# Kernel optimization log

Measured on AMD Instinct MI355X. Metric: run time of the kernel, lower is better.

The kernel has to match this reference:

```python
import jax, jax.numpy as jnp
import numpy as np

EMB_DIM = 1024
NUM_HEADS = 16
HEAD_DIM = EMB_DIM // NUM_HEADS


def _theta_vector(head_dim):
    # theta_i = 10000^(-2i/head_dim), i = 0..head_dim/2-1 (standard RoPE)
    i = jnp.arange(head_dim // 2, dtype=jnp.float32)
    return jnp.power(10000.0, -2.0 * i / head_dim)


def _apply_rope(x, cos, sin):
    # x: [B,S,H,D]; cos,sin: [B,S,1,D/2]. Pairwise 2x2 rotation per dim-pair.
    B, S, H, D = x.shape
    xp = x.reshape(B, S, H, D // 2, 2)
    x0, x1 = xp[..., 0], xp[..., 1]
    r0 = x0 * cos - x1 * sin
    r1 = x0 * sin + x1 * cos
    return jnp.stack([r0, r1], axis=-1).reshape(B, S, H, D)


def setup_inputs() -> dict:
    key = jax.random.key(0)
    ks = jax.random.split(key, 11)
    B, S = 2, 2048
    sc = 1.0 / np.sqrt(EMB_DIM)
    x = jax.random.normal(ks[0], (B, S, EMB_DIM), dtype=jnp.float32)
    positions = jnp.sort(jax.random.randint(ks[1], (B, S), 0, 8192), axis=-1)
    Wq = jax.random.normal(ks[2], (EMB_DIM, EMB_DIM), dtype=jnp.float32) * sc
    bq = jax.random.normal(ks[3], (EMB_DIM,), dtype=jnp.float32) * 0.01
    Wk = jax.random.normal(ks[4], (EMB_DIM, EMB_DIM), dtype=jnp.float32) * sc
    bk = jax.random.normal(ks[5], (EMB_DIM,), dtype=jnp.float32) * 0.01
    Wv = jax.random.normal(ks[6], (EMB_DIM, EMB_DIM), dtype=jnp.float32) * sc
    bv = jax.random.normal(ks[7], (EMB_DIM,), dtype=jnp.float32) * 0.01
    Wo = jax.random.normal(ks[8], (EMB_DIM, EMB_DIM), dtype=jnp.float32) * sc
    bo = jax.random.normal(ks[9], (EMB_DIM,), dtype=jnp.float32) * 0.01
    return {"x": x, "positions": positions, "Wq": Wq, "bq": bq, "Wk": Wk,
            "bk": bk, "Wv": Wv, "bv": bv, "Wo": Wo, "bo": bo}


def reference(x, positions, Wq, bq, Wk, bk, Wv, bv, Wo, bo):
    B, S, E = x.shape
    H, D = NUM_HEADS, HEAD_DIM
    Q = (x @ Wq + bq).reshape(B, S, H, D)
    K = (x @ Wk + bk).reshape(B, S, H, D)
    V = (x @ Wv + bv).reshape(B, S, H, D)
    theta = _theta_vector(D)                       # [D/2]
    ang = positions.astype(jnp.float32)[..., None] * theta  # [B,S,D/2]
    cos = jnp.cos(ang)[:, :, None, :]              # [B,S,1,D/2]
    sin = jnp.sin(ang)[:, :, None, :]
    Qr = _apply_rope(Q, cos, sin).transpose(0, 2, 1, 3)   # [B,H,S,D]
    Kr = _apply_rope(K, cos, sin).transpose(0, 2, 1, 3)
    Vh = V.transpose(0, 2, 1, 3)
    scores = jnp.einsum('bhqd,bhkd->bhqk', Qr, Kr) / jnp.sqrt(jnp.float32(D))
    probs = jax.nn.softmax(scores, axis=-1)
    ctx = jnp.einsum('bhqk,bhkd->bhqd', probs, Vh)
    ctx = ctx.transpose(0, 2, 1, 3).reshape(B, S, E)
    return ctx @ Wo + bo
```

## Files before the change

kernel.cpp:

```cpp
#include <hip/hip_runtime.h>
#include <hip/hip_bf16.h>
#include <math.h>

#define B_ 2
#define S_ 2048
#define E_ 1024
#define H_ 16
#define D_ 64
#define M_ 4096
#define NT2 32
#define KVB 64

typedef __bf16 bf16;
typedef __bf16 bf16x4 __attribute__((ext_vector_type(4)));
typedef __bf16 bf16x8 __attribute__((ext_vector_type(8)));
typedef float f32x4 __attribute__((ext_vector_type(4)));
typedef float f32x16 __attribute__((ext_vector_type(16)));

__device__ __forceinline__ void gload_lds16(const void* g, void* lds) {
  __builtin_amdgcn_global_load_lds(
      (const __attribute__((address_space(1))) unsigned int*)g,
      (__attribute__((address_space(3))) unsigned int*)lds, 16, 0, 0);
}

#define MFMA16(a, b, c) __builtin_amdgcn_mfma_f32_16x16x32_bf16(a, b, c, 0, 0, 0)
#define MFMA32(a, b, c) __builtin_amdgcn_mfma_f32_32x32x16_bf16(a, b, c, 0, 0, 0)

__global__ __launch_bounds__(256)
void split_f32_kernel(const float* __restrict__ in, bf16* __restrict__ hi,
                      bf16* __restrict__ lo, int n4) {
  int i = blockIdx.x * 256 + threadIdx.x;
  if (i >= n4) return;
  float4 v = ((const float4*)in)[i];
  bf16 h0 = (bf16)v.x, h1 = (bf16)v.y, h2 = (bf16)v.z, h3 = (bf16)v.w;
  bf16x4 hv = {h0, h1, h2, h3};
  bf16x4 lv = {(bf16)(v.x - (float)h0), (bf16)(v.y - (float)h1),
               (bf16)(v.z - (float)h2), (bf16)(v.w - (float)h3)};
  *(bf16x4*)(hi + 4 * (size_t)i) = hv;
  *(bf16x4*)(lo + 4 * (size_t)i) = lv;
}

__global__ __launch_bounds__(256)
void transpose_split_kernel(const float* __restrict__ W, bf16* __restrict__ Th,
                            bf16* __restrict__ Tl) {
  __shared__ float tile[32][33];
  const int tx = threadIdx.x & 31, ty = threadIdx.x >> 5;
  const int c0 = blockIdx.x * 32, r0 = blockIdx.y * 32;
#pragma unroll
  for (int i = 0; i < 4; ++i)
    tile[ty + 8 * i][tx] = W[(size_t)(r0 + ty + 8 * i) * E_ + c0 + tx];
  __syncthreads();
#pragma unroll
  for (int i = 0; i < 4; ++i) {
    int rr = ty + 8 * i;
    float v = tile[tx][rr];
    bf16 hv = (bf16)v;
    size_t oidx = (size_t)(c0 + rr) * E_ + r0 + tx;
    Th[oidx] = hv;
    Tl[oidx] = (bf16)(v - (float)hv);
  }
}

__global__ __launch_bounds__(256)
void rope_tab_kernel(const int* __restrict__ pos, float* __restrict__ cosT,
                     float* __restrict__ sinT) {
  int idx = blockIdx.x * 256 + threadIdx.x;
  int t = idx & 31, bs = idx >> 5;
  double th = pow(10000.0, -(double)(2 * t) / 64.0);
  float ang = (float)pos[bs] * (float)th;
  double a = (double)ang;
  cosT[idx] = (float)cos(a);
  sinT[idx] = (float)sin(a);
}

#define BMg 128
#define BNg 128
#define BKg 32

__global__ __launch_bounds__(256)
void gemm_qkv_kernel(const bf16* __restrict__ Ah_g, const bf16* __restrict__ Al_g,
                     const bf16* __restrict__ BhQ, const bf16* __restrict__ BlQ,
                     const bf16* __restrict__ BhK, const bf16* __restrict__ BlK,
                     const bf16* __restrict__ BhV, const bf16* __restrict__ BlV,
                     const float* __restrict__ bqp, const float* __restrict__ bkp,
                     const float* __restrict__ bvp,
                     const float* __restrict__ cosT, const float* __restrict__ sinT,
                     bf16* __restrict__ Qh, bf16* __restrict__ Qlo,
                     bf16* __restrict__ Kh, bf16* __restrict__ Klo,
                     bf16* __restrict__ VTb) {
  __shared__ bf16 lA_h[BMg * BKg], lA_l[BMg * BKg];
  __shared__ bf16 lB_h[BNg * BKg], lB_l[BNg * BKg];
  const int tid = threadIdx.x;
  const int nb = blockIdx.x;
  const int third = nb >> 3;
  const int n0 = (nb & 7) * BNg;
  const int m0 = blockIdx.y * BMg;
  const bf16* Bh_g = third == 0 ? BhQ : third == 1 ? BhK : BhV;
  const bf16* Bl_g = third == 0 ? BlQ : third == 1 ? BlK : BlV;
  const float* bias = third == 0 ? bqp : third == 1 ? bkp : bvp;
  const int wave = tid >> 6, lane = tid & 63;
  const int wr = wave >> 1, wc = wave & 1;
  const int r = lane & 31, half = lane >> 5;
  const int KD = 1024;

  f32x16 acc[2][2] = {};

  for (int kt = 0; kt < KD / BKg; ++kt) {
    const int k0 = kt * BKg;
    {
      const bf16* gsrc[4] = {Ah_g, Al_g, Bh_g, Bl_g};
      bf16* ldst[4] = {lA_h, lA_l, lB_h, lB_l};
      const int rs[4] = {m0, m0, n0, n0};
#pragma unroll
      for (int mm = 0; mm < 4; ++mm) {
#pragma unroll
        for (int i = 0; i < 2; ++i) {
          int c = i * 256 + tid;
          int row = c >> 2, u = c & 3;
          int us = u ^ ((row >> 1) & 3);
          const char* gp =
              (const char*)(gsrc[mm] + (size_t)(rs[mm] + row) * KD + k0) + us * 16;
          char* lp = (char*)ldst[mm] + (size_t)(i * 256 + wave * 64) * 16;
          gload_lds16(gp, lp);
        }
      }
    }
    __syncthreads();
#pragma unroll
    for (int ks = 0; ks < 2; ++ks) {
      bf16x8 a_h[2], a_l[2], b_h[2], b_l[2];
#pragma unroll
      for (int mi = 0; mi < 2; ++mi) {
        int row = wr * 64 + mi * 32 + r;
        int boff = row * 64 + ((ks * 32 + half * 16) ^ (((row >> 1) & 3) << 4));
        a_h[mi] = *(const bf16x8*)((const char*)lA_h + boff);
        a_l[mi] = *(const bf16x8*)((const char*)lA_l + boff);
      }
#pragma unroll
      for (int ni = 0; ni < 2; ++ni) {
        int row = wc * 64 + ni * 32 + r;
        int boff = row * 64 + ((ks * 32 + half * 16) ^ (((row >> 1) & 3) << 4));
        b_h[ni] = *(const bf16x8*)((const char*)lB_h + boff);
        b_l[ni] = *(const bf16x8*)((const char*)lB_l + boff);
      }
#pragma unroll
      for (int mi = 0; mi < 2; ++mi)
#pragma unroll
        for (int ni = 0; ni < 2; ++ni) {
          acc[mi][ni] = MFMA32(a_h[mi], b_h[ni], acc[mi][ni]);
          acc[mi][ni] = MFMA32(a_h[mi], b_l[ni], acc[mi][ni]);
          acc[mi][ni] = MFMA32(a_l[mi], b_h[ni], acc[mi][ni]);
        }
    }
    __syncthreads();
  }

#pragma unroll
  for (int mi = 0; mi < 2; ++mi)
#pragma unroll
    for (int ni = 0; ni < 2; ++ni) {
      const int gcol = n0 + wc * 64 + ni * 32 + r;
      const float bv = bias[gcol];
      if (third < 2) {
        bf16* outH = third == 0 ? Qh : Kh;
        bf16* outL = third == 0 ? Qlo : Klo;
        const int h = gcol >> 6, d = gcol & 63, tt = d >> 1;
#pragma unroll
        for (int tq = 0; tq < 4; ++tq) {
#pragma unroll
          for (int u = 0; u < 4; ++u) {
            int reg = tq * 4 + u;
            int grow = m0 + wr * 64 + mi * 32 + (u + 8 * tq + 4 * half);
            int s = grow & (S_ - 1), b = grow >> 11;
            float v = acc[mi][ni][reg] + bv;
            float other = __shfl_xor(v, 1);
            float cs = cosT[(size_t)(b * S_ + s) * NT2 + tt];
            float sn = sinT[(size_t)(b * S_ + s) * NT2 + tt];
            float vr = (d & 1) ? (other * sn + v * cs) : (v * cs - other * sn);
            if (third == 0) vr *= 0.125f;
            bf16 hv = (bf16)vr;
            bf16 lv = (bf16)(vr - (float)hv);
            size_t idx = (((size_t)(b * H_ + h)) * S_ + s) * D_ + d;
            outH[idx] = hv;
            outL[idx] = lv;
          }
        }
      } else {
        const int h = gcol >> 6, d = gcol & 63;
#pragma unroll
        for (int tq = 0; tq < 4; ++tq) {
          int grow = m0 + wr * 64 + mi * 32 + (8 * tq + 4 * half);
          int s = grow & (S_ - 1), b = grow >> 11;
          ushort4 pk;
          unsigned short* pp = (unsigned short*)&pk;
#pragma unroll
          for (int u = 0; u < 4; ++u) {
            float v = acc[mi][ni][tq * 4 + u] + bv;
            bf16 hv = (bf16)v;
            pp[u] = __builtin_bit_cast(unsigned short, hv);
          }
          *(ushort4*)((unsigned short*)VTb +
                      (((size_t)(b * H_ + h)) * D_ + d) * S_ + s) = pk;
        }
      }
    }
}

__global__ __launch_bounds__(256)
void gemm_o_kernel(const bf16* __restrict__ Ah_g, const bf16* __restrict__ Al_g,
                   const bf16* __restrict__ Bh_g, const bf16* __restrict__ Bl_g,
                   const float* __restrict__ bias, float* __restrict__ outF) {
  __shared__ bf16 lA_h[BMg * BKg], lA_l[BMg * BKg];
  __shared__ bf16 lB_h[BNg * BKg], lB_l[BNg * BKg];
  const int tid = threadIdx.x;
  const int m0 = blockIdx.y * BMg, n0 = blockIdx.x * BNg;
  const int wave = tid >> 6, lane = tid & 63;
  const int wr = wave >> 1, wc = wave & 1;
  const int r = lane & 31, half = lane >> 5;
  const int KD = 1024;

  f32x16 acc[2][2] = {};

  for (int kt = 0; kt < KD / BKg; ++kt) {
    const int k0 = kt * BKg;
    {
      const bf16* gsrc[4] = {Ah_g, Al_g, Bh_g, Bl_g};
      bf16* ldst[4] = {lA_h, lA_l, lB_h, lB_l};
      const int rs[4] = {m0, m0, n0, n0};
#pragma unroll
      for (int mm = 0; mm < 4; ++mm) {
#pragma unroll
        for (int i = 0; i < 2; ++i) {
          int c = i * 256 + tid;
          int row = c >> 2, u = c & 3;
          int us = u ^ ((row >> 1) & 3);
          const char* gp =
              (const char*)(gsrc[mm] + (size_t)(rs[mm] + row) * KD + k0) + us * 16;
          char* lp = (char*)ldst[mm] + (size_t)(i * 256 + wave * 64) * 16;
          gload_lds16(gp, lp);
        }
      }
    }
    __syncthreads();
#pragma unroll
    for (int ks = 0; ks < 2; ++ks) {
      bf16x8 a_h[2], a_l[2], b_h[2], b_l[2];
#pragma unroll
      for (int mi = 0; mi < 2; ++mi) {
        int row = wr * 64 + mi * 32 + r;
        int boff = row * 64 + ((ks * 32 + half * 16) ^ (((row >> 1) & 3) << 4));
        a_h[mi] = *(const bf16x8*)((const char*)lA_h + boff);
        a_l[mi] = *(const bf16x8*)((const char*)lA_l + boff);
      }
#pragma unroll
      for (int ni = 0; ni < 2; ++ni) {
        int row = wc * 64 + ni * 32 + r;
        int boff = row * 64 + ((ks * 32 + half * 16) ^ (((row >> 1) & 3) << 4));
        b_h[ni] = *(const bf16x8*)((const char*)lB_h + boff);
        b_l[ni] = *(const bf16x8*)((const char*)lB_l + boff);
      }
#pragma unroll
      for (int mi = 0; mi < 2; ++mi)
#pragma unroll
        for (int ni = 0; ni < 2; ++ni) {
          acc[mi][ni] = MFMA32(a_h[mi], b_h[ni], acc[mi][ni]);
          acc[mi][ni] = MFMA32(a_h[mi], b_l[ni], acc[mi][ni]);
          acc[mi][ni] = MFMA32(a_l[mi], b_h[ni], acc[mi][ni]);
        }
    }
    __syncthreads();
  }

#pragma unroll
  for (int mi = 0; mi < 2; ++mi)
#pragma unroll
    for (int ni = 0; ni < 2; ++ni) {
      const int gcol = n0 + wc * 64 + ni * 32 + r;
      const float bv = bias[gcol];
#pragma unroll
      for (int tq = 0; tq < 4; ++tq)
#pragma unroll
        for (int u = 0; u < 4; ++u) {
          int grow = m0 + wr * 64 + mi * 32 + (u + 8 * tq + 4 * half);
          outF[(size_t)grow * E_ + gcol] = acc[mi][ni][tq * 4 + u] + bv;
        }
    }
}

__global__ __launch_bounds__(256)
void attn_kernel(const bf16* __restrict__ Qh, const bf16* __restrict__ Ql,
                 const bf16* __restrict__ Kh, const bf16* __restrict__ Kl,
                 const bf16* __restrict__ VT, bf16* __restrict__ Ch,
                 bf16* __restrict__ Cl) {
  __shared__ bf16 sKh[2][KVB * 64];
  __shared__ bf16 sKl[2][KVB * 64];
  __shared__ bf16 sV[2][KVB * 64];

  const int tid = threadIdx.x;
  const int wave = tid >> 6, lane = tid & 63;
  const int r = lane & 15, hq = lane >> 4;
  const int bid = blockIdx.x;
  const int swz = (bid & 7) * 64 + (bid >> 3);
  const int bh = swz >> 4, qblk = swz & 15;
  const int q0 = qblk * 128 + wave * 32;
  const size_t hb = (size_t)bh * (S_ * D_);
  const size_t vb = (size_t)bh * (D_ * S_);

  bf16x8 qh[2][2], ql[2][2];
#pragma unroll
  for (int mi = 0; mi < 2; ++mi)
#pragma unroll
    for (int ks = 0; ks < 2; ++ks) {
      size_t off = hb + (size_t)(q0 + mi * 16 + r) * D_ + ks * 32 + hq * 8;
      qh[mi][ks] = *(const bf16x8*)&Qh[off];
      ql[mi][ks] = *(const bf16x8*)&Ql[off];
    }

  float m_lane[2] = {-1e30f, -1e30f};
  float l_lane[2] = {0.f, 0.f};
  f32x4 o[2][4] = {};

  auto stageK = [&](int kt, int buf) {
    const bf16* kbh = Kh + hb + (size_t)kt * (KVB * D_);
    const bf16* kbl = Kl + hb + (size_t)kt * (KVB * D_);
#pragma unroll
    for (int i = 0; i < 2; ++i) {
      int c = i * 256 + tid;
      int ldo = (i * 256 + wave * 64) * 16;
      int cs = c ^ ((c >> 3) & 7);
      gload_lds16(kbh + cs * 8, (char*)&sKh[buf][0] + ldo);
      gload_lds16(kbl + cs * 8, (char*)&sKl[buf][0] + ldo);
    }
  };
  uint4 vld[2];
  auto loadV = [&](int kt) {
    const bf16* vbp = VT + vb + kt * KVB;
#pragma unroll
    for (int i = 0; i < 2; ++i) {
      int c = i * 256 + tid;
      int row = c >> 3, w = c & 7;
      vld[i] = *(const uint4*)(vbp + (size_t)row * S_ + w * 8);
    }
  };
  auto writeV = [&](int buf) {
#pragma unroll
    for (int i = 0; i < 2; ++i) {
      int c = i * 256 + tid;
      int row = c >> 3, w = c & 7;
      int pb0 = (w >> 2) * 32 + (w & 1) * 16 + ((w >> 1) & 1) * 4;
      char* base = (char*)&sV[buf][0] + row * 128;
      uint2 lo = {vld[i].x, vld[i].y};
      uint2 hi = {vld[i].z, vld[i].w};
      *(uint2*)(base + ((pb0 * 2) ^ ((row & 7) << 4))) = lo;
      *(uint2*)(base + (((pb0 + 8) * 2) ^ ((row & 7) << 4))) = hi;
    }
  };

  stageK(0, 0);
  loadV(0);
  writeV(0);
  __syncthreads();
  int cur = 0;

  for (int kt = 0; kt < S_ / KVB; ++kt) {
    if (kt + 1 < S_ / KVB) {
      stageK(kt + 1, cur ^ 1);
      loadV(kt + 1);
    }

    f32x4 sf[2][4] = {};
#pragma unroll
    for (int nf = 0; nf < 4; ++nf)
#pragma unroll
      for (int ks = 0; ks < 2; ++ks) {
        int kk = nf * 16 + r;
        int boff = (kk * 128 + ks * 64 + hq * 16) ^ ((kk & 7) << 4);
        bf16x8 kkh = *(const bf16x8*)((const char*)&sKh[cur][0] + boff);
        bf16x8 kkl = *(const bf16x8*)((const char*)&sKl[cur][0] + boff);
#pragma unroll
        for (int mi = 0; mi < 2; ++mi) {
          sf[mi][nf] = MFMA16(kkh, qh[mi][ks], sf[mi][nf]);
          sf[mi][nf] = MFMA16(kkh, ql[mi][ks], sf[mi][nf]);
          sf[mi][nf] = MFMA16(kkl, qh[mi][ks], sf[mi][nf]);
        }
      }

    float lmax[2];
#pragma unroll
    for (int mi = 0; mi < 2; ++mi) {
      f32x4 m4;
#pragma unroll
      for (int e = 0; e < 4; ++e)
        m4[e] = fmaxf(fmaxf(sf[mi][0][e], sf[mi][1][e]),
                      fmaxf(sf[mi][2][e], sf[mi][3][e]));
      lmax[mi] = fmaxf(fmaxf(m4[0], m4[1]), fmaxf(m4[2], m4[3]));
    }
    int need = (lmax[0] > m_lane[0] + 8.f) || (lmax[1] > m_lane[1] + 8.f);
    if (__any(need)) {
#pragma unroll
      for (int mi = 0; mi < 2; ++mi) {
        float mx = lmax[mi];
        mx = fmaxf(mx, __shfl_xor(mx, 16));
        mx = fmaxf(mx, __shfl_xor(mx, 32));
        float mn = fmaxf(m_lane[mi], mx);
        float al = __expf(m_lane[mi] - mn);
        l_lane[mi] *= al;
        m_lane[mi] = mn;
        int alb = __builtin_bit_cast(int, al);
#pragma unroll
        for (int j = 0; j < 4; ++j) {
          int g = __builtin_amdgcn_ds_bpermute((hq * 4 + j) * 4, alb);
          float a = __builtin_bit_cast(float, g);
#pragma unroll
          for (int nd = 0; nd < 4; ++nd) o[mi][nd][j] *= a;
        }
      }
    }
    bf16x8 pa[2][2];
#pragma unroll
    for (int mi = 0; mi < 2; ++mi) {
      f32x4 s4 = {};
#pragma unroll
      for (int nf = 0; nf < 4; ++nf)
#pragma unroll
        for (int e = 0; e < 4; ++e) {
          float pv = __expf(sf[mi][nf][e] - m_lane[mi]);
          sf[mi][nf][e] = pv;
          s4[e] += pv;
        }
      l_lane[mi] += s4[0] + s4[1] + s4[2] + s4[3];
#pragma unroll
      for (int ks = 0; ks < 2; ++ks) {
        bf16x8 t;
#pragma unroll
        for (int e = 0; e < 4; ++e) {
          t[e] = (bf16)sf[mi][2 * ks][e];
          t[4 + e] = (bf16)sf[mi][2 * ks + 1][e];
        }
        pa[mi][ks] = t;
      }
    }

#pragma unroll
    for (int nd = 0; nd < 4; ++nd)
#pragma unroll
      for (int ks = 0; ks < 2; ++ks) {
        int dd = nd * 16 + r;
        int boff = (dd * 128 + ks * 64 + hq * 16) ^ ((dd & 7) << 4);
        bf16x8 vv = *(const bf16x8*)((const char*)&sV[cur][0] + boff);
#pragma unroll
        for (int mi = 0; mi < 2; ++mi)
          o[mi][nd] = MFMA16(pa[mi][ks], vv, o[mi][nd]);
      }

    if (kt + 1 < S_ / KVB) writeV(cur ^ 1);
    __syncthreads();
    cur ^= 1;
  }

  const int b = bh >> 4, h = bh & 15;
  float lq[2][4];
#pragma unroll
  for (int mi = 0; mi < 2; ++mi) {
    float lr = l_lane[mi];
    lr += __shfl_xor(lr, 16);
    lr += __shfl_xor(lr, 32);
    int lb = __builtin_bit_cast(int, lr);
#pragma unroll
    for (int j = 0; j < 4; ++j) {
      int g = __builtin_amdgcn_ds_bpermute((hq * 4 + j) * 4, lb);
      lq[mi][j] = __builtin_bit_cast(float, g);
    }
  }
#pragma unroll
  for (int mi = 0; mi < 2; ++mi)
#pragma unroll
    for (int nd = 0; nd < 4; ++nd)
#pragma unroll
      for (int j = 0; j < 4; ++j) {
        int s = q0 + mi * 16 + hq * 4 + j;
        int d = nd * 16 + r;
        float ov = o[mi][nd][j] / lq[mi][j];
        bf16 hv = (bf16)ov;
        bf16 lv = (bf16)(ov - (float)hv);
        size_t idx = (((size_t)(b * S_ + s)) * H_ + h) * D_ + d;
        Ch[idx] = hv;
        Cl[idx] = lv;
      }
}

extern "C" void kernel_launch(void* const* d_in, const int* in_sizes, int n_in,
                              void* d_out, int out_size, void* d_ws, size_t ws_size,
                              hipStream_t stream) {
  const float* x = (const float*)d_in[0];
  const int* pos = (const int*)d_in[1];
  const float* Wq = (const float*)d_in[2];
  const float* bq = (const float*)d_in[3];
  const float* Wk = (const float*)d_in[4];
  const float* bk = (const float*)d_in[5];
  const float* Wv = (const float*)d_in[6];
  const float* bv = (const float*)d_in[7];
  const float* Wo = (const float*)d_in[8];
  const float* bo = (const float*)d_in[9];
  float* out = (float*)d_out;

  char* p = (char*)d_ws;
  auto alloc = [&](size_t bytes) {
    char* rp = p;
    p += (bytes + 255) & ~(size_t)255;
    return rp;
  };
  const size_t XB = (size_t)M_ * E_ * sizeof(bf16);
  const size_t WB = (size_t)E_ * E_ * sizeof(bf16);
  const size_t TB = (size_t)B_ * S_ * NT2 * sizeof(float);
  bf16* Xh = (bf16*)alloc(XB);
  bf16* Xl = (bf16*)alloc(XB);
  bf16* WqTh = (bf16*)alloc(WB); bf16* WqTl = (bf16*)alloc(WB);
  bf16* WkTh = (bf16*)alloc(WB); bf16* WkTl = (bf16*)alloc(WB);
  bf16* WvTh = (bf16*)alloc(WB); bf16* WvTl = (bf16*)alloc(WB);
  bf16* WoTh = (bf16*)alloc(WB); bf16* WoTl = (bf16*)alloc(WB);
  float* cosT = (float*)alloc(TB);
  float* sinT = (float*)alloc(TB);
  bf16* Qh = (bf16*)alloc(XB); bf16* Qlo = (bf16*)alloc(XB);
  bf16* Kh = (bf16*)alloc(XB); bf16* Klo = (bf16*)alloc(XB);
  bf16* VTb = (bf16*)alloc(XB);
  bf16* Ch = Xh;
  bf16* Cl = Xl;

  split_f32_kernel<<<M_ * E_ / 4 / 256, 256, 0, stream>>>(x, Xh, Xl, M_ * E_ / 4);
  dim3 tg(32, 32);
  transpose_split_kernel<<<tg, 256, 0, stream>>>(Wq, WqTh, WqTl);
  transpose_split_kernel<<<tg, 256, 0, stream>>>(Wk, WkTh, WkTl);
  transpose_split_kernel<<<tg, 256, 0, stream>>>(Wv, WvTh, WvTl);
  transpose_split_kernel<<<tg, 256, 0, stream>>>(Wo, WoTh, WoTl);
  rope_tab_kernel<<<B_ * S_ * NT2 / 256, 256, 0, stream>>>(pos, cosT, sinT);

  dim3 gq(24, 32);
  gemm_qkv_kernel<<<gq, 256, 0, stream>>>(Xh, Xl, WqTh, WqTl, WkTh, WkTl, WvTh,
                                          WvTl, bq, bk, bv, cosT, sinT, Qh, Qlo,
                                          Kh, Klo, VTb);

  attn_kernel<<<B_ * H_ * (S_ / 128), 256, 0, stream>>>(Qh, Qlo, Kh, Klo, VTb,
                                                        Ch, Cl);

  dim3 go(8, 32);
  gemm_o_kernel<<<go, 256, 0, stream>>>(Ch, Cl, WoTh, WoTl, bo, out);
}
```

Measured before the change: 246.3 us.

## Use 8-wave GEMM blocks, merge weight transposes, add MFMA priority hints

Both GEMM kernels move from 256 to 512 threads per 128x128 tile. Each wave now owns a 64x32 sub-tile, which halves per-wave accumulators and gives the scheduler more waves to hide latency with. The four weight transpose/split launches are merged into one launch indexed by blockIdx.z, cutting launch overhead. s_setprio hints are wrapped around the MFMA sections in the GEMMs and attention. The cost is less B-fragment reuse per wave and more LDS reads per MFMA.

```diff
diff --git a/kernel.cpp b/kernel.cpp
--- a/kernel.cpp
+++ b/kernel.cpp
@@ -41,8 +41,16 @@
 }
 
 __global__ __launch_bounds__(256)
-void transpose_split_kernel(const float* __restrict__ W, bf16* __restrict__ Th,
-                            bf16* __restrict__ Tl) {
+void transpose_split4_kernel(const float* __restrict__ Wq, const float* __restrict__ Wk,
+                             const float* __restrict__ Wv, const float* __restrict__ Wo,
+                             bf16* __restrict__ Tqh, bf16* __restrict__ Tql,
+                             bf16* __restrict__ Tkh, bf16* __restrict__ Tkl,
+                             bf16* __restrict__ Tvh, bf16* __restrict__ Tvl,
+                             bf16* __restrict__ Toh, bf16* __restrict__ Tol) {
+  const int z = blockIdx.z;
+  const float* W = z == 0 ? Wq : z == 1 ? Wk : z == 2 ? Wv : Wo;
+  bf16* Th = z == 0 ? Tqh : z == 1 ? Tkh : z == 2 ? Tvh : Toh;
+  bf16* Tl = z == 0 ? Tql : z == 1 ? Tkl : z == 2 ? Tvl : Tol;
   __shared__ float tile[32][33];
   const int tx = threadIdx.x & 31, ty = threadIdx.x >> 5;
   const int c0 = blockIdx.x * 32, r0 = blockIdx.y * 32;
@@ -77,7 +85,7 @@
 #define BNg 128
 #define BKg 32
 
-__global__ __launch_bounds__(256)
+__global__ __launch_bounds__(512, 4)
 void gemm_qkv_kernel(const bf16* __restrict__ Ah_g, const bf16* __restrict__ Al_g,
                      const bf16* __restrict__ BhQ, const bf16* __restrict__ BlQ,
                      const bf16* __restrict__ BhK, const bf16* __restrict__ BlK,
@@ -99,11 +107,11 @@
   const bf16* Bl_g = third == 0 ? BlQ : third == 1 ? BlK : BlV;
   const float* bias = third == 0 ? bqp : third == 1 ? bkp : bvp;
   const int wave = tid >> 6, lane = tid & 63;
-  const int wr = wave >> 1, wc = wave & 1;
+  const int wr = wave >> 2, wc = wave & 3;
   const int r = lane & 31, half = lane >> 5;
   const int KD = 1024;
 
-  f32x16 acc[2][2] = {};
+  f32x16 acc[2] = {};
 
   for (int kt = 0; kt < KD / BKg; ++kt) {
     const int k0 = kt * BKg;
@@ -113,22 +121,19 @@
       const int rs[4] = {m0, m0, n0, n0};
 #pragma unroll
       for (int mm = 0; mm < 4; ++mm) {
-#pragma unroll
-        for (int i = 0; i < 2; ++i) {
-          int c = i * 256 + tid;
-          int row = c >> 2, u = c & 3;
-          int us = u ^ ((row >> 1) & 3);
-          const char* gp =
-              (const char*)(gsrc[mm] + (size_t)(rs[mm] + row) * KD + k0) + us * 16;
-          char* lp = (char*)ldst[mm] + (size_t)(i * 256 + wave * 64) * 16;
-          gload_lds16(gp, lp);
-        }
+        int c = tid;
+        int row = c >> 2, u = c & 3;
+        int us = u ^ ((row >> 1) & 3);
+        const char* gp =
+            (const char*)(gsrc[mm] + (size_t)(rs[mm] + row) * KD + k0) + us * 16;
+        char* lp = (char*)ldst[mm] + (size_t)(wave * 64) * 16;
+        gload_lds16(gp, lp);
       }
     }
     __syncthreads();
 #pragma unroll
     for (int ks = 0; ks < 2; ++ks) {
-      bf16x8 a_h[2], a_l[2], b_h[2], b_l[2];
+      bf16x8 a_h[2], a_l[2], b_h, b_l;
 #pragma unroll
       for (int mi = 0; mi < 2; ++mi) {
         int row = wr * 64 + mi * 32 + r;
@@ -136,77 +141,74 @@
         a_h[mi] = *(const bf16x8*)((const char*)lA_h + boff);
         a_l[mi] = *(const bf16x8*)((const char*)lA_l + boff);
       }
-#pragma unroll
-      for (int ni = 0; ni < 2; ++ni) {
-        int row = wc * 64 + ni * 32 + r;
+      {
+        int row = wc * 32 + r;
         int boff = row * 64 + ((ks * 32 + half * 16) ^ (((row >> 1) & 3) << 4));
-        b_h[ni] = *(const bf16x8*)((const char*)lB_h + boff);
-        b_l[ni] = *(const bf16x8*)((const char*)lB_l + boff);
-      }
-#pragma unroll
-      for (int mi = 0; mi < 2; ++mi)
-#pragma unroll
-        for (int ni = 0; ni < 2; ++ni) {
-          acc[mi][ni] = MFMA32(a_h[mi], b_h[ni], acc[mi][ni]);
-          acc[mi][ni] = MFMA32(a_h[mi], b_l[ni], acc[mi][ni]);
-          acc[mi][ni] = MFMA32(a_l[mi], b_h[ni], acc[mi][ni]);
+        b_h = *(const bf16x8*)((const char*)lB_h + boff);
+        b_l = *(const bf16x8*)((const char*)lB_l + boff);
+      }
+      __builtin_amdgcn_s_setprio(1);
+#pragma unroll
+      for (int mi = 0; mi < 2; ++mi) {
+        acc[mi] = MFMA32(a_h[mi], b_h, acc[mi]);
+        acc[mi] = MFMA32(a_h[mi], b_l, acc[mi]);
+        acc[mi] = MFMA32(a_l[mi], b_h, acc[mi]);
+      }
+      __builtin_amdgcn_s_setprio(0);
+    }
+    __syncthreads();
+  }
+
+#pragma unroll
+  for (int mi = 0; mi < 2; ++mi) {
+    const int gcol = n0 + wc * 32 + r;
+    const float bv = bias[gcol];
+    if (third < 2) {
+      bf16* outH = third == 0 ? Qh : Kh;
+      bf16* outL = third == 0 ? Qlo : Klo;
+      const int h = gcol >> 6, d = gcol & 63, tt = d >> 1;
+#pragma unroll
+      for (int tq = 0; tq < 4; ++tq) {
+#pragma unroll
+        for (int u = 0; u < 4; ++u) {
+          int reg = tq * 4 + u;
+          int grow = m0 + wr * 64 + mi * 32 + (u + 8 * tq + 4 * half);
+          int s = grow & (S_ - 1), b = grow >> 11;
+          float v = acc[mi][reg] + bv;
+          float other = __shfl_xor(v, 1);
+          float cs = cosT[(size_t)(b * S_ + s) * NT2 + tt];
+          float sn = sinT[(size_t)(b * S_ + s) * NT2 + tt];
+          float vr = (d & 1) ? (other * sn + v * cs) : (v * cs - other * sn);
+          if (third == 0) vr *= 0.125f;
+          bf16 hv = (bf16)vr;
+          bf16 lv = (bf16)(vr - (float)hv);
+          size_t idx = (((size_t)(b * H_ + h)) * S_ + s) * D_ + d;
+          outH[idx] = hv;
+          outL[idx] = lv;
         }
-    }
-    __syncthreads();
-  }
-
-#pragma unroll
-  for (int mi = 0; mi < 2; ++mi)
-#pragma unroll
-    for (int ni = 0; ni < 2; ++ni) {
-      const int gcol = n0 + wc * 64 + ni * 32 + r;
-      const float bv = bias[gcol];
-      if (third < 2) {
-        bf16* outH = third == 0 ? Qh : Kh;
-        bf16* outL = third == 0 ? Qlo : Klo;
-        const int h = gcol >> 6, d = gcol & 63, tt = d >> 1;
-#pragma unroll
-        for (int tq = 0; tq < 4; ++tq) {
-#pragma unroll
-          for (int u = 0; u < 4; ++u) {
-            int reg = tq * 4 + u;
-            int grow = m0 + wr * 64 + mi * 32 + (u + 8 * tq + 4 * half);
-            int s = grow & (S_ - 1), b = grow >> 11;
-            float v = acc[mi][ni][reg] + bv;
-            float other = __shfl_xor(v, 1);
-            float cs = cosT[(size_t)(b * S_ + s) * NT2 + tt];
-            float sn = sinT[(size_t)(b * S_ + s) * NT2 + tt];
-            float vr = (d & 1) ? (other * sn + v * cs) : (v * cs - other * sn);
-            if (third == 0) vr *= 0.125f;
-            bf16 hv = (bf16)vr;
-            bf16 lv = (bf16)(vr - (float)hv);
-            size_t idx = (((size_t)(b * H_ + h)) * S_ + s) * D_ + d;
-            outH[idx] = hv;
-            outL[idx] = lv;
-          }
+      }
+    } else {
+      const int h = gcol >> 6, d = gcol & 63;
+#pragma unroll
+      for (int tq = 0; tq < 4; ++tq) {
+        int grow = m0 + wr * 64 + mi * 32 + (8 * tq + 4 * half);
+        int s = grow & (S_ - 1), b = grow >> 11;
+        ushort4 pk;
+        unsigned short* pp = (unsigned short*)&pk;
+#pragma unroll
+        for (int u = 0; u < 4; ++u) {
+          float v = acc[mi][tq * 4 + u] + bv;
+          bf16 hv = (bf16)v;
+          pp[u] = __builtin_bit_cast(unsigned short, hv);
         }
-      } else {
-        const int h = gcol >> 6, d = gcol & 63;
-#pragma unroll
-        for (int tq = 0; tq < 4; ++tq) {
-          int grow = m0 + wr * 64 + mi * 32 + (8 * tq + 4 * half);
-          int s = grow & (S_ - 1), b = grow >> 11;
-          ushort4 pk;
-          unsigned short* pp = (unsigned short*)&pk;
-#pragma unroll
-          for (int u = 0; u < 4; ++u) {
-            float v = acc[mi][ni][tq * 4 + u] + bv;
-            bf16 hv = (bf16)v;
-            pp[u] = __builtin_bit_cast(unsigned short, hv);
-          }
-          *(ushort4*)((unsigned short*)VTb +
-                      (((size_t)(b * H_ + h)) * D_ + d) * S_ + s) = pk;
-        }
-      }
-    }
-}
-
-__global__ __launch_bounds__(256)
+        *(ushort4*)((unsigned short*)VTb +
+                    (((size_t)(b * H_ + h)) * D_ + d) * S_ + s) = pk;
+      }
+    }
+  }
+}
+
+__global__ __launch_bounds__(512, 4)
 void gemm_o_kernel(const bf16* __restrict__ Ah_g, const bf16* __restrict__ Al_g,
                    const bf16* __restrict__ Bh_g, const bf16* __restrict__ Bl_g,
                    const float* __restrict__ bias, float* __restrict__ outF) {
@@ -215,11 +217,11 @@
   const int tid = threadIdx.x;
   const int m0 = blockIdx.y * BMg, n0 = blockIdx.x * BNg;
   const int wave = tid >> 6, lane = tid & 63;
-  const int wr = wave >> 1, wc = wave & 1;
+  const int wr = wave >> 2, wc = wave & 3;
   const int r = lane & 31, half = lane >> 5;
   const int KD = 1024;
 
-  f32x16 acc[2][2] = {};
+  f32x16 acc[2] = {};
 
   for (int kt = 0; kt < KD / BKg; ++kt) {
     const int k0 = kt * BKg;
@@ -229,22 +231,19 @@
       const int rs[4] = {m0, m0, n0, n0};
 #pragma unroll
       for (int mm = 0; mm < 4; ++mm) {
-#pragma unroll
-        for (int i = 0; i < 2; ++i) {
-          int c = i * 256 + tid;
-          int row = c >> 2, u = c & 3;
-          int us = u ^ ((row >> 1) & 3);
-          const char* gp =
-              (const char*)(gsrc[mm] + (size_t)(rs[mm] + row) * KD + k0) + us * 16;
-          char* lp = (char*)ldst[mm] + (size_t)(i * 256 + wave * 64) * 16;
-          gload_lds16(gp, lp);
-        }
+        int c = tid;
+        int row = c >> 2, u = c & 3;
+        int us = u ^ ((row >> 1) & 3);
+        const char* gp =
+            (const char*)(gsrc[mm] + (size_t)(rs[mm] + row) * KD + k0) + us * 16;
+        char* lp = (char*)ldst[mm] + (size_t)(wave * 64) * 16;
+        gload_lds16(gp, lp);
       }
     }
     __syncthreads();
 #pragma unroll
     for (int ks = 0; ks < 2; ++ks) {
-      bf16x8 a_h[2], a_l[2], b_h[2], b_l[2];
+      bf16x8 a_h[2], a_l[2], b_h, b_l;
 #pragma unroll
       for (int mi = 0; mi < 2; ++mi) {
         int row = wr * 64 + mi * 32 + r;
@@ -252,39 +251,36 @@
         a_h[mi] = *(const bf16x8*)((const char*)lA_h + boff);
         a_l[mi] = *(const bf16x8*)((const char*)lA_l + boff);
       }
-#pragma unroll
-      for (int ni = 0; ni < 2; ++ni) {
-        int row = wc * 64 + ni * 32 + r;
+      {
+        int row = wc * 32 + r;
         int boff = row * 64 + ((ks * 32 + half * 16) ^ (((row >> 1) & 3) << 4));
-        b_h[ni] = *(const bf16x8*)((const char*)lB_h + boff);
-        b_l[ni] = *(const bf16x8*)((const char*)lB_l + boff);
-      }
-#pragma unroll
-      for (int mi = 0; mi < 2; ++mi)
-#pragma unroll
-        for (int ni = 0; ni < 2; ++ni) {
-          acc[mi][ni] = MFMA32(a_h[mi], b_h[ni], acc[mi][ni]);
-          acc[mi][ni] = MFMA32(a_h[mi], b_l[ni], acc[mi][ni]);
-          acc[mi][ni] = MFMA32(a_l[mi], b_h[ni], acc[mi][ni]);
-        }
+        b_h = *(const bf16x8*)((const char*)lB_h + boff);
+        b_l = *(const bf16x8*)((const char*)lB_l + boff);
+      }
+      __builtin_amdgcn_s_setprio(1);
+#pragma unroll
+      for (int mi = 0; mi < 2; ++mi) {
+        acc[mi] = MFMA32(a_h[mi], b_h, acc[mi]);
+        acc[mi] = MFMA32(a_h[mi], b_l, acc[mi]);
+        acc[mi] = MFMA32(a_l[mi], b_h, acc[mi]);
+      }
+      __builtin_amdgcn_s_setprio(0);
     }
     __syncthreads();
   }
 
 #pragma unroll
-  for (int mi = 0; mi < 2; ++mi)
-#pragma unroll
-    for (int ni = 0; ni < 2; ++ni) {
-      const int gcol = n0 + wc * 64 + ni * 32 + r;
-      const float bv = bias[gcol];
-#pragma unroll
-      for (int tq = 0; tq < 4; ++tq)
-#pragma unroll
-        for (int u = 0; u < 4; ++u) {
-          int grow = m0 + wr * 64 + mi * 32 + (u + 8 * tq + 4 * half);
-          outF[(size_t)grow * E_ + gcol] = acc[mi][ni][tq * 4 + u] + bv;
-        }
-    }
+  for (int mi = 0; mi < 2; ++mi) {
+    const int gcol = n0 + wc * 32 + r;
+    const float bv = bias[gcol];
+#pragma unroll
+    for (int tq = 0; tq < 4; ++tq)
+#pragma unroll
+      for (int u = 0; u < 4; ++u) {
+        int grow = m0 + wr * 64 + mi * 32 + (u + 8 * tq + 4 * half);
+        outF[(size_t)grow * E_ + gcol] = acc[mi][tq * 4 + u] + bv;
+      }
+  }
 }
 
 __global__ __launch_bounds__(256)
@@ -369,6 +365,7 @@
     }
 
     f32x4 sf[2][4] = {};
+    __builtin_amdgcn_s_setprio(1);
 #pragma unroll
     for (int nf = 0; nf < 4; ++nf)
 #pragma unroll
@@ -384,6 +381,7 @@
           sf[mi][nf] = MFMA16(kkl, qh[mi][ks], sf[mi][nf]);
         }
       }
+    __builtin_amdgcn_s_setprio(0);
 
     float lmax[2];
 #pragma unroll
@@ -441,6 +439,7 @@
       }
     }
 
+    __builtin_amdgcn_s_setprio(1);
 #pragma unroll
     for (int nd = 0; nd < 4; ++nd)
 #pragma unroll
@@ -452,6 +451,7 @@
         for (int mi = 0; mi < 2; ++mi)
           o[mi][nd] = MFMA16(pa[mi][ks], vv, o[mi][nd]);
       }
+    __builtin_amdgcn_s_setprio(0);
 
     if (kt + 1 < S_ / KVB) writeV(cur ^ 1);
     __syncthreads();
@@ -528,15 +528,14 @@
   bf16* Cl = Xl;
 
   split_f32_kernel<<<M_ * E_ / 4 / 256, 256, 0, stream>>>(x, Xh, Xl, M_ * E_ / 4);
-  dim3 tg(32, 32);
-  transpose_split_kernel<<<tg, 256, 0, stream>>>(Wq, WqTh, WqTl);
-  transpose_split_kernel<<<tg, 256, 0, stream>>>(Wk, WkTh, WkTl);
-  transpose_split_kernel<<<tg, 256, 0, stream>>>(Wv, WvTh, WvTl);
-  transpose_split_kernel<<<tg, 256, 0, stream>>>(Wo, WoTh, WoTl);
+  dim3 tg(32, 32, 4);
+  transpose_split4_kernel<<<tg, 256, 0, stream>>>(Wq, Wk, Wv, Wo, WqTh, WqTl,
+                                                  WkTh, WkTl, WvTh, WvTl, WoTh,
+                                                  WoTl);
   rope_tab_kernel<<<B_ * S_ * NT2 / 256, 256, 0, stream>>>(pos, cosT, sinT);
 
   dim3 gq(24, 32);
-  gemm_qkv_kernel<<<gq, 256, 0, stream>>>(Xh, Xl, WqTh, WqTl, WkTh, WkTl, WvTh,
+  gemm_qkv_kernel<<<gq, 512, 0, stream>>>(Xh, Xl, WqTh, WqTl, WkTh, WkTl, WvTh,
                                           WvTl, bq, bk, bv, cosT, sinT, Qh, Qlo,
                                           Kh, Klo, VTb);
 
@@ -544,5 +543,5 @@
                                                         Ch, Cl);
 
   dim3 go(8, 32);
-  gemm_o_kernel<<<go, 256, 0, stream>>>(Ch, Cl, WoTh, WoTl, bo, out);
-}
+  gemm_o_kernel<<<go, 512, 0, stream>>>(Ch, Cl, WoTh, WoTl, bo, out);
+}
```

After: 240.4 us. 2.4% less time.
